# Kernel optimization log

Hardware: AMD Instinct MI355X
Metric: run time of the kernel (lower is better)

Reference implementation:

```python
import jax, jax.numpy as jnp
from jax import lax
import numpy as np

NOTES = 78
IN_DIM = 80
T_HID = 64
N_HID = 2
B = 64
T = 128


def lstm_seq(x, w_ih, w_hh, b_ih, b_hh):
    """Batch-first single-layer LSTM from zero state.
    x: (N, S, D); w_ih: (4H, D); w_hh: (4H, H). Gate order i,f,g,o (PyTorch).
    Returns hidden outputs (N, S, H)."""
    H = w_hh.shape[1]
    N = x.shape[0]
    # precompute input contribution for all steps: (N, S, 4H)
    gx = jnp.einsum('nsd,gd->nsg', x, w_ih) + b_ih + b_hh

    def step(carry, g_t):
        h, c = carry
        g = g_t + h @ w_hh.T
        i, f, gg, o = jnp.split(g, 4, axis=-1)
        c = jax.nn.sigmoid(f) * c + jax.nn.sigmoid(i) * jnp.tanh(gg)
        h = jax.nn.sigmoid(o) * jnp.tanh(c)
        return (h, c), h

    h0 = jnp.zeros((N, H), x.dtype)
    (_, _), hs = lax.scan(step, (h0, h0), jnp.swapaxes(gx, 0, 1))
    return jnp.swapaxes(hs, 0, 1)  # (N, S, H)


def setup_inputs() -> dict:
    key = jax.random.key(0)
    ks = jax.random.split(key, 9)
    s = 1.0 / np.sqrt(T_HID)
    sn = 1.0 / np.sqrt(N_HID)
    u = lambda k, shp, sc: jax.random.uniform(k, shp, jnp.float32, -sc, sc)
    return {
        'x': jax.random.normal(ks[0], (B, NOTES, T, IN_DIM), jnp.float32),
        'w_ih_t': u(ks[1], (4 * T_HID, IN_DIM), s),
        'w_hh_t': u(ks[2], (4 * T_HID, T_HID), s),
        'b_ih_t': u(ks[3], (4 * T_HID,), s),
        'b_hh_t': u(ks[4], (4 * T_HID,), s),
        'w_ih_n': u(ks[5], (4 * N_HID, T_HID), sn),
        'w_hh_n': u(ks[6], (4 * N_HID, N_HID), sn),
        'b_ih_n': u(ks[7], (4 * N_HID,), sn),
        'b_hh_n': u(ks[8], (4 * N_HID,), sn),
    }


def reference(x, w_ih_t, w_hh_t, b_ih_t, b_hh_t, w_ih_n, w_hh_n, b_ih_n, b_hh_n):
    b, n_notes, t_len, _ = x.shape
    # Time LSTM: independent over (batch, note); sequence axis = time.
    xt = x.reshape(b * n_notes, t_len, IN_DIM)
    time_out = lstm_seq(xt, w_ih_t, w_hh_t, b_ih_t, b_hh_t)  # (B*78, T, H)
    time_out = time_out.reshape(b, n_notes, t_len, T_HID)
    # Note LSTM: run over the 78-note axis, fresh zero state at EVERY time step
    # (faithful to the original, which reuses self.hidden_note0 each iteration).
    xn = jnp.transpose(time_out, (0, 2, 1, 3)).reshape(b * t_len, n_notes, T_HID)
    note_out = lstm_seq(xn, w_ih_n, w_hh_n, b_ih_n, b_hh_n)  # (B*T, 78, 2)
    note_out = note_out.reshape(b, t_len, n_notes * N_HID)  # (B, T, 156)
    # Hard threshold, exactly as torch.where(x > 0.5, ones, zeros)
    return jnp.where(note_out > 0.5, jnp.ones_like(note_out), jnp.zeros_like(note_out))
```

## Files before the change

### kernel.cpp

```cpp
#include <hip/hip_runtime.h>
#include <math.h>

#define NOTES 78
#define IN_DIM 80
#define T_HID 64
#define N_HID 2
#define BATCH 64
#define TLEN 128
#define NSEQ (BATCH * NOTES)
#define NBT  (BATCH * TLEN)
#define SB   4

__device__ __forceinline__ float sigf(float x) { return 1.0f / (1.0f + expf(-x)); }
__device__ __forceinline__ float rdl(float v, int k) {
    return __int_as_float(__builtin_amdgcn_readlane(__float_as_int(v), k));
}

__global__ __launch_bounds__(256, 2)
void time_lstm_fused(const float* __restrict__ x,
                     const float* __restrict__ w_ih,
                     const float* __restrict__ w_hh,
                     const float* __restrict__ b_ih,
                     const float* __restrict__ b_hh,
                     const float* __restrict__ w_ih_n,
                     const float* __restrict__ b_ih_n,
                     const float* __restrict__ b_hh_n,
                     float* __restrict__ gxn) {
    __shared__ float hbuf[SB][T_HID];
    __shared__ float G0[SB][256];
    __shared__ float G1[SB][256];

    const int tid  = threadIdx.x;
    const int s0   = blockIdx.x * SB;
    const int wid  = tid >> 6;
    const int lane = tid & 63;
    const bool isx = (wid < 2);
    const int g0   = ((wid & 1) << 7) | (2 * lane);

    float4 wA[20], wB[20];
    float biasA = 0.0f, biasB = 0.0f;
    if (isx) {
        const float4* pA = (const float4*)(w_ih + (size_t)g0 * IN_DIM);
        const float4* pB = (const float4*)(w_ih + (size_t)(g0 + 1) * IN_DIM);
#pragma unroll
        for (int j = 0; j < 20; j++) { wA[j] = pA[j]; wB[j] = pB[j]; }
        biasA = b_ih[g0] + b_hh[g0];
        biasB = b_ih[g0 + 1] + b_hh[g0 + 1];
    } else {
        const float4* pA = (const float4*)(w_hh + (size_t)g0 * T_HID);
        const float4* pB = (const float4*)(w_hh + (size_t)(g0 + 1) * T_HID);
#pragma unroll
        for (int j = 0; j < 16; j++) { wA[j] = pA[j]; wB[j] = pB[j]; }
    }

    const float* xr[SB];
#pragma unroll
    for (int s = 0; s < SB; s++) xr[s] = x + (size_t)(s0 + s) * TLEN * IN_DIM;

    float xa[SB], xb[SB];
    if (isx) {
#pragma unroll
        for (int s = 0; s < SB; s++) {
            xa[s] = xr[s][lane];
            xb[s] = xr[s][64 + (lane & 15)];
        }
    }

    float cst = 0.0f;

    const int su2 = tid >> 6;
    const int nj  = (tid >> 3) & 7;
    const int nk  = tid & 7;
    float wn[8];
#pragma unroll
    for (int i = 0; i < 8; i++) wn[i] = w_ih_n[nj * 64 + nk * 8 + i];
    const float nbias = b_ih_n[nj] + b_hh_n[nj];
    const int sglb = s0 + su2;
    const int nb = sglb / NOTES, nn = sglb % NOTES;
    float* gout = gxn + ((size_t)nn * NBT + (size_t)nb * TLEN) * 8 + nj;

    hbuf[wid][lane] = 0.0f;
    __syncthreads();

    for (int t = 0; t < TLEN; t++) {
        if (t > 0) {
            float p = 0.0f;
#pragma unroll
            for (int i = 0; i < 8; i++) p = fmaf(wn[i], hbuf[su2][nk * 8 + i], p);
            p += __shfl_xor(p, 1);
            p += __shfl_xor(p, 2);
            p += __shfl_xor(p, 4);
            if (nk == 0) gout[(size_t)(t - 1) * 8] = p + nbias;
        }

        float xna[SB], xnb[SB];
        const bool pf = isx && (t + 1 < TLEN);
        if (pf) {
#pragma unroll
            for (int s = 0; s < SB; s++) {
                xna[s] = xr[s][(t + 1) * IN_DIM + lane];
                xnb[s] = xr[s][(t + 1) * IN_DIM + 64 + (lane & 15)];
            }
        }

        if (isx) {
            float aA[SB], aB[SB];
#pragma unroll
            for (int s = 0; s < SB; s++) { aA[s] = biasA; aB[s] = biasB; }
#pragma unroll
            for (int k4 = 0; k4 < 16; k4++) {
                const float4 vA = wA[k4], vB = wB[k4];
#pragma unroll
                for (int s = 0; s < SB; s++) {
                    const float r0 = rdl(xa[s], 4 * k4 + 0);
                    const float r1 = rdl(xa[s], 4 * k4 + 1);
                    const float r2 = rdl(xa[s], 4 * k4 + 2);
                    const float r3 = rdl(xa[s], 4 * k4 + 3);
                    aA[s] = fmaf(vA.x, r0, aA[s]);  aB[s] = fmaf(vB.x, r0, aB[s]);
                    aA[s] = fmaf(vA.y, r1, aA[s]);  aB[s] = fmaf(vB.y, r1, aB[s]);
                    aA[s] = fmaf(vA.z, r2, aA[s]);  aB[s] = fmaf(vB.z, r2, aB[s]);
                    aA[s] = fmaf(vA.w, r3, aA[s]);  aB[s] = fmaf(vB.w, r3, aB[s]);
                }
            }
#pragma unroll
            for (int k4 = 16; k4 < 20; k4++) {
                const float4 vA = wA[k4], vB = wB[k4];
#pragma unroll
                for (int s = 0; s < SB; s++) {
                    const float r0 = rdl(xb[s], 4 * k4 - 64);
                    const float r1 = rdl(xb[s], 4 * k4 - 63);
                    const float r2 = rdl(xb[s], 4 * k4 - 62);
                    const float r3 = rdl(xb[s], 4 * k4 - 61);
                    aA[s] = fmaf(vA.x, r0, aA[s]);  aB[s] = fmaf(vB.x, r0, aB[s]);
                    aA[s] = fmaf(vA.y, r1, aA[s]);  aB[s] = fmaf(vB.y, r1, aB[s]);
                    aA[s] = fmaf(vA.z, r2, aA[s]);  aB[s] = fmaf(vB.z, r2, aB[s]);
                    aA[s] = fmaf(vA.w, r3, aA[s]);  aB[s] = fmaf(vB.w, r3, aB[s]);
                }
            }
#pragma unroll
            for (int s = 0; s < SB; s++) {
                *(float2*)&G0[s][g0] = make_float2(aA[s], aB[s]);
            }
        } else {
            float hv[SB];
#pragma unroll
            for (int s = 0; s < SB; s++) hv[s] = hbuf[s][lane];
            float aA[SB], aB[SB];
#pragma unroll
            for (int s = 0; s < SB; s++) { aA[s] = 0.0f; aB[s] = 0.0f; }
#pragma unroll
            for (int k4 = 0; k4 < 16; k4++) {
                const float4 vA = wA[k4], vB = wB[k4];
#pragma unroll
                for (int s = 0; s < SB; s++) {
                    const float r0 = rdl(hv[s], 4 * k4 + 0);
                    const float r1 = rdl(hv[s], 4 * k4 + 1);
                    const float r2 = rdl(hv[s], 4 * k4 + 2);
                    const float r3 = rdl(hv[s], 4 * k4 + 3);
                    aA[s] = fmaf(vA.x, r0, aA[s]);  aB[s] = fmaf(vB.x, r0, aB[s]);
                    aA[s] = fmaf(vA.y, r1, aA[s]);  aB[s] = fmaf(vB.y, r1, aB[s]);
                    aA[s] = fmaf(vA.z, r2, aA[s]);  aB[s] = fmaf(vB.z, r2, aB[s]);
                    aA[s] = fmaf(vA.w, r3, aA[s]);  aB[s] = fmaf(vB.w, r3, aB[s]);
                }
            }
#pragma unroll
            for (int s = 0; s < SB; s++) {
                *(float2*)&G1[s][g0] = make_float2(aA[s], aB[s]);
            }
        }
        __syncthreads();

        {
            const float i_p = G0[wid][lane]       + G1[wid][lane];
            const float f_p = G0[wid][64 + lane]  + G1[wid][64 + lane];
            const float g_p = G0[wid][128 + lane] + G1[wid][128 + lane];
            const float o_p = G0[wid][192 + lane] + G1[wid][192 + lane];
            cst = sigf(f_p) * cst + sigf(i_p) * tanhf(g_p);
            const float h = sigf(o_p) * tanhf(cst);
            hbuf[wid][lane] = h;
        }
        if (pf) {
#pragma unroll
            for (int s = 0; s < SB; s++) { xa[s] = xna[s]; xb[s] = xnb[s]; }
        }
        __syncthreads();
    }

    {
        float p = 0.0f;
#pragma unroll
        for (int i = 0; i < 8; i++) p = fmaf(wn[i], hbuf[su2][nk * 8 + i], p);
        p += __shfl_xor(p, 1);
        p += __shfl_xor(p, 2);
        p += __shfl_xor(p, 4);
        if (nk == 0) gout[(size_t)(TLEN - 1) * 8] = p + nbias;
    }
}

__global__ __launch_bounds__(64)
void note_scan_kernel(const float* __restrict__ gxn,
                      const float* __restrict__ w_hh_n,
                      float* __restrict__ out) {
    const int bt = blockIdx.x * 64 + threadIdx.x;
    float wh[16];
#pragma unroll
    for (int i = 0; i < 16; i++) wh[i] = w_hh_n[i];
    float h0 = 0.f, h1 = 0.f, c0 = 0.f, c1 = 0.f;

    const float4* gp = (const float4*)gxn;
    float res[2 * NOTES];

    size_t idx = (size_t)bt * 2;
    float4 ga = gp[idx], gb = gp[idx + 1];
    for (int n = 0; n < NOTES; n++) {
        float4 na, nb2;
        if (n + 1 < NOTES) {
            const size_t nidx = ((size_t)(n + 1) * NBT + bt) * 2;
            na  = gp[nidx];
            nb2 = gp[nidx + 1];
        }
        const float i0 = ga.x + wh[0]  * h0 + wh[1]  * h1;
        const float i1 = ga.y + wh[2]  * h0 + wh[3]  * h1;
        const float f0 = ga.z + wh[4]  * h0 + wh[5]  * h1;
        const float f1 = ga.w + wh[6]  * h0 + wh[7]  * h1;
        const float g0 = gb.x + wh[8]  * h0 + wh[9]  * h1;
        const float g1 = gb.y + wh[10] * h0 + wh[11] * h1;
        const float o0 = gb.z + wh[12] * h0 + wh[13] * h1;
        const float o1 = gb.w + wh[14] * h0 + wh[15] * h1;
        c0 = sigf(f0) * c0 + sigf(i0) * tanhf(g0);
        c1 = sigf(f1) * c1 + sigf(i1) * tanhf(g1);
        h0 = sigf(o0) * tanhf(c0);
        h1 = sigf(o1) * tanhf(c1);
        res[n * 2 + 0] = (h0 > 0.5f) ? 1.0f : 0.0f;
        res[n * 2 + 1] = (h1 > 0.5f) ? 1.0f : 0.0f;
        ga = na; gb = nb2;
    }
    float4* op = (float4*)(out + (size_t)bt * (NOTES * N_HID));
#pragma unroll
    for (int j = 0; j < (2 * NOTES) / 4; j++) {
        op[j] = make_float4(res[4 * j], res[4 * j + 1], res[4 * j + 2], res[4 * j + 3]);
    }
}

extern "C" void kernel_launch(void* const* d_in, const int* in_sizes, int n_in,
                              void* d_out, int out_size, void* d_ws, size_t ws_size,
                              hipStream_t stream) {
    const float* x      = (const float*)d_in[0];
    const float* w_ih_t = (const float*)d_in[1];
    const float* w_hh_t = (const float*)d_in[2];
    const float* b_ih_t = (const float*)d_in[3];
    const float* b_hh_t = (const float*)d_in[4];
    const float* w_ih_n = (const float*)d_in[5];
    const float* w_hh_n = (const float*)d_in[6];
    const float* b_ih_n = (const float*)d_in[7];
    const float* b_hh_n = (const float*)d_in[8];
    float* out = (float*)d_out;

    float* gxn = (float*)d_ws;

    time_lstm_fused<<<NSEQ / SB, 256, 0, stream>>>(
        x, w_ih_t, w_hh_t, b_ih_t, b_hh_t, w_ih_n, b_ih_n, b_hh_n, gxn);
    note_scan_kernel<<<NBT / 64, 64, 0, stream>>>(gxn, w_hh_n, out);
}
```

Measured before the change: 1.352 ms.

## Give each thread one full gate row, double sequences per block

Restructures the time LSTM so each of 256 threads owns one gate row and computes both its input and recurrent contributions. Previously two waves did input and two did recurrent work, each for two gates. The block now processes 8 sequences instead of 4, merges the two gate buffers into one, and applies the sigmoid/tanh per gate before the cell update. This removes the G0+G1 summation and halves the number of blocks. It raises per-thread register pressure (36 float4 weights plus 8-sequence accumulators) and adds more serial FMA work per thread.

```diff
diff --git a/kernel.cpp b/kernel.cpp
--- a/kernel.cpp
+++ b/kernel.cpp
@@ -9,14 +9,14 @@
 #define TLEN 128
 #define NSEQ (BATCH * NOTES)
 #define NBT  (BATCH * TLEN)
-#define SB   4
+#define SB   8
 
 __device__ __forceinline__ float sigf(float x) { return 1.0f / (1.0f + expf(-x)); }
 __device__ __forceinline__ float rdl(float v, int k) {
     return __int_as_float(__builtin_amdgcn_readlane(__float_as_int(v), k));
 }
 
-__global__ __launch_bounds__(256, 2)
+__global__ __launch_bounds__(256) __attribute__((amdgpu_waves_per_eu(2, 2)))
 void time_lstm_fused(const float* __restrict__ x,
                      const float* __restrict__ w_ih,
                      const float* __restrict__ w_hh,
@@ -27,161 +27,139 @@
                      const float* __restrict__ b_hh_n,
                      float* __restrict__ gxn) {
     __shared__ float hbuf[SB][T_HID];
-    __shared__ float G0[SB][256];
-    __shared__ float G1[SB][256];
+    __shared__ float G[SB][256];
 
     const int tid  = threadIdx.x;
     const int s0   = blockIdx.x * SB;
-    const int wid  = tid >> 6;
+    const int g    = tid;
     const int lane = tid & 63;
-    const bool isx = (wid < 2);
-    const int g0   = ((wid & 1) << 7) | (2 * lane);
-
-    float4 wA[20], wB[20];
-    float biasA = 0.0f, biasB = 0.0f;
-    if (isx) {
-        const float4* pA = (const float4*)(w_ih + (size_t)g0 * IN_DIM);
-        const float4* pB = (const float4*)(w_ih + (size_t)(g0 + 1) * IN_DIM);
-#pragma unroll
-        for (int j = 0; j < 20; j++) { wA[j] = pA[j]; wB[j] = pB[j]; }
-        biasA = b_ih[g0] + b_hh[g0];
-        biasB = b_ih[g0 + 1] + b_hh[g0 + 1];
-    } else {
-        const float4* pA = (const float4*)(w_hh + (size_t)g0 * T_HID);
-        const float4* pB = (const float4*)(w_hh + (size_t)(g0 + 1) * T_HID);
-#pragma unroll
-        for (int j = 0; j < 16; j++) { wA[j] = pA[j]; wB[j] = pB[j]; }
-    }
+    const int gtype = tid >> 6;
+
+    float4 wih[20], whh[16];
+    {
+        const float4* p = (const float4*)(w_ih + (size_t)g * IN_DIM);
+#pragma unroll
+        for (int j = 0; j < 20; j++) wih[j] = p[j];
+        const float4* q = (const float4*)(w_hh + (size_t)g * T_HID);
+#pragma unroll
+        for (int j = 0; j < 16; j++) whh[j] = q[j];
+    }
+    const float bias = b_ih[g] + b_hh[g];
 
     const float* xr[SB];
 #pragma unroll
     for (int s = 0; s < SB; s++) xr[s] = x + (size_t)(s0 + s) * TLEN * IN_DIM;
 
-    float xa[SB], xb[SB];
-    if (isx) {
-#pragma unroll
-        for (int s = 0; s < SB; s++) {
-            xa[s] = xr[s][lane];
-            xb[s] = xr[s][64 + (lane & 15)];
-        }
-    }
-
-    float cst = 0.0f;
-
-    const int su2 = tid >> 6;
-    const int nj  = (tid >> 3) & 7;
-    const int nk  = tid & 7;
-    float wn[8];
-#pragma unroll
-    for (int i = 0; i < 8; i++) wn[i] = w_ih_n[nj * 64 + nk * 8 + i];
+    const int su2 = tid >> 5;
+    const int nj  = (tid >> 2) & 7;
+    const int nk  = tid & 3;
+    float wn[16];
+#pragma unroll
+    for (int i = 0; i < 16; i++) wn[i] = w_ih_n[nj * 64 + nk * 16 + i];
     const float nbias = b_ih_n[nj] + b_hh_n[nj];
     const int sglb = s0 + su2;
     const int nb = sglb / NOTES, nn = sglb % NOTES;
     float* gout = gxn + ((size_t)nn * NBT + (size_t)nb * TLEN) * 8 + nj;
 
-    hbuf[wid][lane] = 0.0f;
+    const int u  = lane;
+    const int sA = tid >> 6;
+    const int sB = sA + 4;
+    float c0 = 0.0f, c1 = 0.0f;
+
+    ((float*)hbuf)[tid] = 0.0f;
+    ((float*)hbuf)[tid + 256] = 0.0f;
+    float xa[SB];
+#pragma unroll
+    for (int s = 0; s < SB; s++) xa[s] = xr[s][lane];
     __syncthreads();
 
     for (int t = 0; t < TLEN; t++) {
+        float xb[SB], hv[SB], xna[SB];
+#pragma unroll
+        for (int s = 0; s < SB; s++) xb[s] = xr[s][t * IN_DIM + 64 + (lane & 15)];
+#pragma unroll
+        for (int s = 0; s < SB; s++) hv[s] = hbuf[s][lane];
+        const bool pf = (t + 1 < TLEN);
+        if (pf) {
+#pragma unroll
+            for (int s = 0; s < SB; s++) xna[s] = xr[s][(t + 1) * IN_DIM + lane];
+        }
+
         if (t > 0) {
             float p = 0.0f;
 #pragma unroll
-            for (int i = 0; i < 8; i++) p = fmaf(wn[i], hbuf[su2][nk * 8 + i], p);
+            for (int i = 0; i < 16; i++)
+                p = fmaf(wn[i], hbuf[su2][nk * 16 + i], p);
             p += __shfl_xor(p, 1);
             p += __shfl_xor(p, 2);
-            p += __shfl_xor(p, 4);
             if (nk == 0) gout[(size_t)(t - 1) * 8] = p + nbias;
         }
 
-        float xna[SB], xnb[SB];
-        const bool pf = isx && (t + 1 < TLEN);
+        float acc[SB];
+#pragma unroll
+        for (int s = 0; s < SB; s++) acc[s] = bias;
+#pragma unroll
+        for (int k4 = 0; k4 < 16; k4++) {
+            const float4 wv = wih[k4];
+#pragma unroll
+            for (int s = 0; s < SB; s++) {
+                const float r0 = rdl(xa[s], 4 * k4 + 0);
+                const float r1 = rdl(xa[s], 4 * k4 + 1);
+                const float r2 = rdl(xa[s], 4 * k4 + 2);
+                const float r3 = rdl(xa[s], 4 * k4 + 3);
+                acc[s] = fmaf(wv.w, r3, fmaf(wv.z, r2,
+                         fmaf(wv.y, r1, fmaf(wv.x, r0, acc[s]))));
+            }
+        }
+#pragma unroll
+        for (int k4 = 16; k4 < 20; k4++) {
+            const float4 wv = wih[k4];
+#pragma unroll
+            for (int s = 0; s < SB; s++) {
+                const float r0 = rdl(xb[s], 4 * k4 - 64);
+                const float r1 = rdl(xb[s], 4 * k4 - 63);
+                const float r2 = rdl(xb[s], 4 * k4 - 62);
+                const float r3 = rdl(xb[s], 4 * k4 - 61);
+                acc[s] = fmaf(wv.w, r3, fmaf(wv.z, r2,
+                         fmaf(wv.y, r1, fmaf(wv.x, r0, acc[s]))));
+            }
+        }
+#pragma unroll
+        for (int k4 = 0; k4 < 16; k4++) {
+            const float4 wv = whh[k4];
+#pragma unroll
+            for (int s = 0; s < SB; s++) {
+                const float r0 = rdl(hv[s], 4 * k4 + 0);
+                const float r1 = rdl(hv[s], 4 * k4 + 1);
+                const float r2 = rdl(hv[s], 4 * k4 + 2);
+                const float r3 = rdl(hv[s], 4 * k4 + 3);
+                acc[s] = fmaf(wv.w, r3, fmaf(wv.z, r2,
+                         fmaf(wv.y, r1, fmaf(wv.x, r0, acc[s]))));
+            }
+        }
+
+#pragma unroll
+        for (int s = 0; s < SB; s++) {
+            const float v = (gtype == 2) ? tanhf(acc[s]) : sigf(acc[s]);
+            G[s][g] = v;
+        }
+        __syncthreads();
+
+        {
+            const float iv = G[sA][u], fv = G[sA][64 + u];
+            const float gv = G[sA][128 + u], ov = G[sA][192 + u];
+            c0 = fv * c0 + iv * gv;
+            hbuf[sA][u] = ov * tanhf(c0);
+        }
+        {
+            const float iv = G[sB][u], fv = G[sB][64 + u];
+            const float gv = G[sB][128 + u], ov = G[sB][192 + u];
+            c1 = fv * c1 + iv * gv;
+            hbuf[sB][u] = ov * tanhf(c1);
+        }
         if (pf) {
 #pragma unroll
-            for (int s = 0; s < SB; s++) {
-                xna[s] = xr[s][(t + 1) * IN_DIM + lane];
-                xnb[s] = xr[s][(t + 1) * IN_DIM + 64 + (lane & 15)];
-            }
-        }
-
-        if (isx) {
-            float aA[SB], aB[SB];
-#pragma unroll
-            for (int s = 0; s < SB; s++) { aA[s] = biasA; aB[s] = biasB; }
-#pragma unroll
-            for (int k4 = 0; k4 < 16; k4++) {
-                const float4 vA = wA[k4], vB = wB[k4];
-#pragma unroll
-                for (int s = 0; s < SB; s++) {
-                    const float r0 = rdl(xa[s], 4 * k4 + 0);
-                    const float r1 = rdl(xa[s], 4 * k4 + 1);
-                    const float r2 = rdl(xa[s], 4 * k4 + 2);
-                    const float r3 = rdl(xa[s], 4 * k4 + 3);
-                    aA[s] = fmaf(vA.x, r0, aA[s]);  aB[s] = fmaf(vB.x, r0, aB[s]);
-                    aA[s] = fmaf(vA.y, r1, aA[s]);  aB[s] = fmaf(vB.y, r1, aB[s]);
-                    aA[s] = fmaf(vA.z, r2, aA[s]);  aB[s] = fmaf(vB.z, r2, aB[s]);
-                    aA[s] = fmaf(vA.w, r3, aA[s]);  aB[s] = fmaf(vB.w, r3, aB[s]);
-                }
-            }
-#pragma unroll
-            for (int k4 = 16; k4 < 20; k4++) {
-                const float4 vA = wA[k4], vB = wB[k4];
-#pragma unroll
-                for (int s = 0; s < SB; s++) {
-                    const float r0 = rdl(xb[s], 4 * k4 - 64);
-                    const float r1 = rdl(xb[s], 4 * k4 - 63);
-                    const float r2 = rdl(xb[s], 4 * k4 - 62);
-                    const float r3 = rdl(xb[s], 4 * k4 - 61);
-                    aA[s] = fmaf(vA.x, r0, aA[s]);  aB[s] = fmaf(vB.x, r0, aB[s]);
-                    aA[s] = fmaf(vA.y, r1, aA[s]);  aB[s] = fmaf(vB.y, r1, aB[s]);
-                    aA[s] = fmaf(vA.z, r2, aA[s]);  aB[s] = fmaf(vB.z, r2, aB[s]);
-                    aA[s] = fmaf(vA.w, r3, aA[s]);  aB[s] = fmaf(vB.w, r3, aB[s]);
-                }
-            }
-#pragma unroll
-            for (int s = 0; s < SB; s++) {
-                *(float2*)&G0[s][g0] = make_float2(aA[s], aB[s]);
-            }
-        } else {
-            float hv[SB];
-#pragma unroll
-            for (int s = 0; s < SB; s++) hv[s] = hbuf[s][lane];
-            float aA[SB], aB[SB];
-#pragma unroll
-            for (int s = 0; s < SB; s++) { aA[s] = 0.0f; aB[s] = 0.0f; }
-#pragma unroll
-            for (int k4 = 0; k4 < 16; k4++) {
-                const float4 vA = wA[k4], vB = wB[k4];
-#pragma unroll
-                for (int s = 0; s < SB; s++) {
-                    const float r0 = rdl(hv[s], 4 * k4 + 0);
-                    const float r1 = rdl(hv[s], 4 * k4 + 1);
-                    const float r2 = rdl(hv[s], 4 * k4 + 2);
-                    const float r3 = rdl(hv[s], 4 * k4 + 3);
-                    aA[s] = fmaf(vA.x, r0, aA[s]);  aB[s] = fmaf(vB.x, r0, aB[s]);
-                    aA[s] = fmaf(vA.y, r1, aA[s]);  aB[s] = fmaf(vB.y, r1, aB[s]);
-                    aA[s] = fmaf(vA.z, r2, aA[s]);  aB[s] = fmaf(vB.z, r2, aB[s]);
-                    aA[s] = fmaf(vA.w, r3, aA[s]);  aB[s] = fmaf(vB.w, r3, aB[s]);
-                }
-            }
-#pragma unroll
-            for (int s = 0; s < SB; s++) {
-                *(float2*)&G1[s][g0] = make_float2(aA[s], aB[s]);
-            }
-        }
-        __syncthreads();
-
-        {
-            const float i_p = G0[wid][lane]       + G1[wid][lane];
-            const float f_p = G0[wid][64 + lane]  + G1[wid][64 + lane];
-            const float g_p = G0[wid][128 + lane] + G1[wid][128 + lane];
-            const float o_p = G0[wid][192 + lane] + G1[wid][192 + lane];
-            cst = sigf(f_p) * cst + sigf(i_p) * tanhf(g_p);
-            const float h = sigf(o_p) * tanhf(cst);
-            hbuf[wid][lane] = h;
-        }
-        if (pf) {
-#pragma unroll
-            for (int s = 0; s < SB; s++) { xa[s] = xna[s]; xb[s] = xnb[s]; }
+            for (int s = 0; s < SB; s++) xa[s] = xna[s];
         }
         __syncthreads();
     }
@@ -189,10 +167,10 @@
     {
         float p = 0.0f;
 #pragma unroll
-        for (int i = 0; i < 8; i++) p = fmaf(wn[i], hbuf[su2][nk * 8 + i], p);
+        for (int i = 0; i < 16; i++)
+            p = fmaf(wn[i], hbuf[su2][nk * 16 + i], p);
         p += __shfl_xor(p, 1);
         p += __shfl_xor(p, 2);
-        p += __shfl_xor(p, 4);
         if (nk == 0) gout[(size_t)(TLEN - 1) * 8] = p + nbias;
     }
 }
```

After: 4.883 ms. +261.3%, slower.
